# Kernel optimization log

Measured on AMD Instinct MI355X. Metric: run time of the kernel, lower is better.

Reference implementation:

```python
import jax, jax.numpy as jnp
import numpy as np

D = 64        # inner_feature_len (dim)
HID = 128     # hidden_channels of the edge MLP
NCONV = 2     # n_conv
STEPS = 3     # Set2Set processing_steps
NSEG = 128    # number of graphs in the batch


def setup_inputs() -> dict:
    key = jax.random.key(0)
    ks = jax.random.split(key, 30)
    N, E, FN, FE = 10000, 64000, 92, 41
    s = 0.05
    p = lambda i, shape: jax.random.normal(ks[i], shape, jnp.float32) * s
    return {
        "x": jax.random.normal(ks[0], (N, FN), jnp.float32),
        "edge_attr": jax.random.uniform(ks[1], (E, FE), dtype=jnp.float32),
        "lin0_w": p(2, (D, FN)), "lin0_b": p(3, (D,)),
        "nn1_w": p(4, (HID, FE)), "nn1_b": p(5, (HID,)),
        "nn2_w": p(6, (D * D, HID)), "nn2_b": p(7, (D * D,)),
        "root_w": p(8, (D, D)), "conv_b": p(9, (D,)),
        "gru_w_ih": p(10, (3 * D, D)), "gru_w_hh": p(11, (3 * D, D)),
        "gru_b_ih": p(12, (3 * D,)), "gru_b_hh": p(13, (3 * D,)),
        "lstm_w_ih": p(14, (4 * D, 2 * D)), "lstm_w_hh": p(15, (4 * D, D)),
        "lstm_b_ih": p(16, (4 * D,)), "lstm_b_hh": p(17, (4 * D,)),
        "lin1_w": p(18, (D, 2 * D)), "lin1_b": p(19, (D,)),
        "lin2_w": p(20, (1, D)), "lin2_b": p(21, (1,)),
        "edge_index": jax.random.randint(ks[22], (2, E), 0, N, dtype=jnp.int32),
        "batch": jnp.sort(jax.random.randint(ks[23], (N,), 0, NSEG, dtype=jnp.int32)),
    }


def _gru_step(m, h, w_ih, w_hh, b_ih, b_hh):
    # torch GRU gate order: r, z, n
    gi = m @ w_ih.T + b_ih
    gh = h @ w_hh.T + b_hh
    r = jax.nn.sigmoid(gi[:, :D] + gh[:, :D])
    z = jax.nn.sigmoid(gi[:, D:2 * D] + gh[:, D:2 * D])
    n = jnp.tanh(gi[:, 2 * D:] + r * gh[:, 2 * D:])
    return (1.0 - z) * n + z * h


def _forward(x, edge_attr, lin0_w, lin0_b, nn1_w, nn1_b, nn2_w, nn2_b, root_w, conv_b,
             gru_w_ih, gru_w_hh, gru_b_ih, gru_b_hh, lstm_w_ih, lstm_w_hh, lstm_b_ih,
             lstm_b_hh, lin1_w, lin1_b, lin2_w, lin2_b, edge_index, batch):
    N = x.shape[0]
    src, dst = edge_index[0], edge_index[1]

    # Edge-conditioned weight matrices: [E, D, D] (dominant intermediate)
    We = (jax.nn.relu(edge_attr @ nn1_w.T + nn1_b) @ nn2_w.T + nn2_b).reshape(-1, D, D)
    deg = jnp.clip(jax.ops.segment_sum(jnp.ones_like(src, jnp.float32), dst, num_segments=N), 1.0, None)

    out = jax.nn.relu(x @ lin0_w.T + lin0_b)   # [N, D]
    h = out                                     # GRU hidden (num_layers=1)
    for _ in range(NCONV):
        # NNConv: gather -> per-edge matmul -> scatter-mean, plus root transform + bias
        msg = jnp.einsum('ei,eio->eo', out[src], We)                 # [E, D]
        agg = jax.ops.segment_sum(msg, dst, num_segments=N) / deg[:, None]
        m = jax.nn.relu(agg + out @ root_w.T + conv_b)
        h = _gru_step(m, h, gru_w_ih, gru_w_hh, gru_b_ih, gru_b_hh)
        out = h

    # Set2Set pooling (LSTM-attention readout)
    q_star = jnp.zeros((NSEG, 2 * D), x.dtype)
    hl = jnp.zeros((NSEG, D), x.dtype)
    cl = jnp.zeros((NSEG, D), x.dtype)
    for _ in range(STEPS):
        g = q_star @ lstm_w_ih.T + lstm_b_ih + hl @ lstm_w_hh.T + lstm_b_hh
        i = jax.nn.sigmoid(g[:, :D])
        f = jax.nn.sigmoid(g[:, D:2 * D])
        gg = jnp.tanh(g[:, 2 * D:3 * D])
        o = jax.nn.sigmoid(g[:, 3 * D:])
        cl = f * cl + i * gg
        hl = o * jnp.tanh(cl)
        q = hl                                   # [NSEG, D]
        e = jnp.sum(out * q[batch], axis=-1)     # [N]
        mmax = jax.ops.segment_max(e, batch, num_segments=NSEG)
        a = jnp.exp(e - mmax[batch])
        denom = jax.ops.segment_sum(a, batch, num_segments=NSEG)
        a = a / denom[batch]
        r = jax.ops.segment_sum(a[:, None] * out, batch, num_segments=NSEG)  # [NSEG, D]
        q_star = jnp.concatenate([q, r], axis=1)

    y = jax.nn.relu(q_star @ lin1_w.T + lin1_b) @ lin2_w.T + lin2_b
    return y.reshape(-1)


def reference(x, edge_attr, lin0_w, lin0_b, nn1_w, nn1_b, nn2_w, nn2_b, root_w, conv_b,
              gru_w_ih, gru_w_hh, gru_b_ih, gru_b_hh, lstm_w_ih, lstm_w_hh, lstm_b_ih,
              lstm_b_hh, lin1_w, lin1_b, lin2_w, lin2_b, edge_index, batch):
    return _forward(x, edge_attr, lin0_w, lin0_b, nn1_w, nn1_b, nn2_w, nn2_b, root_w,
                    conv_b, gru_w_ih, gru_w_hh, gru_b_ih, gru_b_hh, lstm_w_ih, lstm_w_hh,
                    lstm_b_ih, lstm_b_hh, lin1_w, lin1_b, lin2_w, lin2_b, edge_index, batch)
```

## Files before the change

kernel.cpp:

```cpp
#include <hip/hip_runtime.h>
#include <hip/hip_bf16.h>
#include <math.h>

#define DD 64
#define HIDC 128
#define FN 92
#define FE 41
#define S2CAP 192

typedef unsigned short u16;
typedef short bf16x8 __attribute__((ext_vector_type(8)));
typedef float f32x4 __attribute__((ext_vector_type(4)));
typedef u16 u16x8 __attribute__((ext_vector_type(8)));

__device__ __forceinline__ float sigmoidf_(float x){ return 1.f/(1.f+expf(-x)); }

__device__ __forceinline__ u16 f2bf(float v){
  union { float f; unsigned u; } x; x.f = v;
  unsigned r = x.u + 0x7fff + ((x.u >> 16) & 1);
  return (u16)(r >> 16);
}
__device__ __forceinline__ float bf2f(u16 v){
  union { float f; unsigned u; } x; x.u = ((unsigned)v) << 16;
  return x.f;
}
__device__ __forceinline__ void split_bf(float v, u16& h, u16& l){
  h = f2bf(v); l = f2bf(v - bf2f(h));
}

__global__ void k_pack(const float* __restrict__ lin0_w, const float* __restrict__ nn1_w,
                       const float* __restrict__ root_w, const float* __restrict__ gwih,
                       const float* __restrict__ gwhh, const float* __restrict__ lwih,
                       const float* __restrict__ lwhh, const float* __restrict__ lin1_w,
                       float* __restrict__ lin0T, float* __restrict__ nn1T,
                       float* __restrict__ rootT, float* __restrict__ wihT,
                       float* __restrict__ whhT, float* __restrict__ lwihT,
                       float* __restrict__ lwhhT, float* __restrict__ lin1T)
{
  int idx = blockIdx.x*blockDim.x + threadIdx.x;
  if (idx < 92*64){ int k=idx/64, o=idx%64; lin0T[k*64+o] = lin0_w[o*92+k]; return; } idx -= 92*64;
  if (idx < 41*128){ int k=idx/128, h=idx%128; nn1T[k*128+h] = nn1_w[h*41+k]; return; } idx -= 41*128;
  if (idx < 64*64){ int i=idx/64, o=idx%64; rootT[i*64+o] = root_w[o*64+i]; return; } idx -= 64*64;
  if (idx < 64*192){ int i=idx/192, g=idx%192; wihT[i*192+g] = gwih[g*64+i]; return; } idx -= 64*192;
  if (idx < 64*192){ int i=idx/192, g=idx%192; whhT[i*192+g] = gwhh[g*64+i]; return; } idx -= 64*192;
  if (idx < 128*256){ int j=idx/256, t=idx%256; lwihT[j*256+t] = lwih[t*128+j]; return; } idx -= 128*256;
  if (idx < 64*256){ int j=idx/256, t=idx%256; lwhhT[j*256+t] = lwhh[t*64+j]; return; } idx -= 64*256;
  if (idx < 128*64){ int j=idx/64, t=idx%64; lin1T[j*64+t] = lin1_w[t*128+j]; return; }
}

__global__ void k_pack_b2(const float* __restrict__ nn2_w,
                          u16* __restrict__ BhT, u16* __restrict__ BlT){
  int idx = blockIdx.x*256 + threadIdx.x;
  if (idx >= 524288) return;
  int i  = idx & 63;
  int ho = (idx >> 6) & 4095;
  int c  = idx >> 18;
  int h = ho >> 6, o = ho & 63;
  float v = nn2_w[(size_t)(i*64+o)*128 + c*64 + h];
  u16 hi, lo; split_bf(v, hi, lo);
  BhT[idx] = hi; BlT[idx] = lo;
}

__global__ void k_pack_b1(const float* __restrict__ nn1_w,
                          u16* __restrict__ BT1h, u16* __restrict__ BT1l){
  int idx = blockIdx.x*256 + threadIdx.x;
  if (idx >= 8192) return;
  int h = idx >> 6, k = idx & 63;
  float v = (k < FE) ? nn1_w[(size_t)h*FE + k] : 0.f;
  u16 hi, lo; split_bf(v, hi, lo);
  BT1h[idx] = hi; BT1l[idx] = lo;
}

__global__ void k_split_ea(const float* __restrict__ ea, const int* __restrict__ sortedE,
                           u16* __restrict__ eaH, u16* __restrict__ eaL, int E){
  int idx = blockIdx.x*256 + threadIdx.x;
  if (idx >= E*64) return;
  int ew = idx >> 6, k = idx & 63;
  int e = sortedE[ew];
  float v = (k < FE) ? ea[(size_t)e*FE + k] : 0.f;
  u16 hi, lo; split_bf(v, hi, lo);
  eaH[idx] = hi; eaL[idx] = lo;
}

__global__ __launch_bounds__(256) void k_node_mlp(const float* __restrict__ x,
    const float* __restrict__ lin0T, const float* __restrict__ lin0_b,
    const float* __restrict__ nn2_b,
    float* __restrict__ out, u16* __restrict__ outH, u16* __restrict__ outL,
    float* __restrict__ bterm, int N)
{
  __shared__ float xs[4][FN];
  int base = blockIdx.x*4;
  for (int i=threadIdx.x; i<4*FN; i+=256){
    int n = base + i/FN;
    xs[i/FN][i%FN] = (n<N) ? x[(size_t)n*FN + i%FN] : 0.f;
  }
  __syncthreads();
  int ln = threadIdx.x>>6, o = threadIdx.x&63;
  int n = base+ln;
  if (n>=N) return;
  float acc = lin0_b[o];
  #pragma unroll 4
  for (int k=0;k<FN;k++) acc = fmaf(xs[ln][k], lin0T[k*64+o], acc);
  float v = fmaxf(acc, 0.f);
  out[(size_t)n*64+o] = v;
  u16 hi, lo; split_bf(v, hi, lo);
  outH[(size_t)n*64+o] = hi;
  outL[(size_t)n*64+o] = lo;
  float bt = 0.f;
  #pragma unroll 8
  for (int i=0;i<64;i++) bt = fmaf(__shfl(v, i, 64), nn2_b[i*64+o], bt);
  bterm[(size_t)n*64+o] = bt;
}

__global__ void k_count(const int* __restrict__ dst, const int* __restrict__ src,
                        float* __restrict__ deg, int* __restrict__ scnt, int E){
  int e = blockIdx.x*blockDim.x + threadIdx.x;
  if (e < E){
    atomicAdd(&deg[dst[e]], 1.f);
    atomicAdd(&scnt[src[e]], 1);
  }
}

__global__ void k_scan1(const int* __restrict__ cnt, int* __restrict__ excl,
                        int* __restrict__ bsum, int N){
  __shared__ int buf[256];
  int i = blockIdx.x*256 + threadIdx.x;
  int v = (i<N) ? cnt[i] : 0;
  buf[threadIdx.x] = v;
  __syncthreads();
  #pragma unroll
  for (int off=1; off<256; off<<=1){
    int t = (threadIdx.x>=off) ? buf[threadIdx.x-off] : 0;
    __syncthreads();
    buf[threadIdx.x] += t;
    __syncthreads();
  }
  if (i<N) excl[i] = buf[threadIdx.x] - v;
  if (threadIdx.x==255) bsum[blockIdx.x] = buf[255];
}
__global__ void k_scan2(int* __restrict__ bsum, int nb){
  __shared__ int buf[256];
  int v = (threadIdx.x<nb) ? bsum[threadIdx.x] : 0;
  buf[threadIdx.x] = v;
  __syncthreads();
  #pragma unroll
  for (int off=1; off<256; off<<=1){
    int t = (threadIdx.x>=off) ? buf[threadIdx.x-off] : 0;
    __syncthreads();
    buf[threadIdx.x] += t;
    __syncthreads();
  }
  if (threadIdx.x<nb) bsum[threadIdx.x] = buf[threadIdx.x] - v;
}
__global__ void k_scan3(int* __restrict__ starts, int* __restrict__ cursor,
                        const int* __restrict__ bsum, int N, int E){
  int i = blockIdx.x*256 + threadIdx.x;
  if (i<N){
    int s = starts[i] + bsum[blockIdx.x];
    starts[i] = s;
    cursor[i] = s;
  }
  if (i==0) starts[N] = E;
}

__global__ void k_sort(const int* __restrict__ src, const int* __restrict__ dst,
                       int* __restrict__ cursor, int* __restrict__ sortedE,
                       int* __restrict__ srcS, int* __restrict__ dstS, int E){
  int e = blockIdx.x*256 + threadIdx.x;
  if (e < E){
    int s = src[e];
    int p = atomicAdd(&cursor[s], 1);
    sortedE[p] = e;
    srcS[p] = s;
    dstS[p] = dst[e];
  }
}

__global__ __launch_bounds__(256,3) void k_edge_mlp_mfma(
    const u16* __restrict__ eaH, const u16* __restrict__ eaL,
    const u16* __restrict__ BT1h, const u16* __restrict__ BT1l,
    const float* __restrict__ nn1_b, float* __restrict__ hidden, int E)
{
  const int lane = threadIdx.x & 63;
  const int wave = threadIdx.x >> 6;
  const int row  = lane & 15;
  const int quad = lane >> 4;
  const int m0 = blockIdx.x*128 + (wave>>1)*64;
  const int n0 = (wave&1)*64;

  bf16x8 AH0[4], AH1[4], AL0[4], AL1[4];
  #pragma unroll
  for (int p=0;p<4;p++){
    int ar = min(m0 + p*16 + row, E-1);
    const u16* aH = eaH + (size_t)ar*64 + quad*8;
    const u16* aL = eaL + (size_t)ar*64 + quad*8;
    AH0[p] = *(const bf16x8*)(aH);
    AH1[p] = *(const bf16x8*)(aH + 32);
    AL0[p] = *(const bf16x8*)(aL);
    AL1[p] = *(const bf16x8*)(aL + 32);
  }
  #pragma unroll
  for (int tb=0;tb<4;tb++){
    const u16* bH = BT1h + (size_t)(n0 + tb*16 + row)*64 + quad*8;
    const u16* bL = BT1l + (size_t)(n0 + tb*16 + row)*64 + quad*8;
    bf16x8 bh0 = *(const bf16x8*)(bH);
    bf16x8 bh1 = *(const bf16x8*)(bH + 32);
    bf16x8 bl0 = *(const bf16x8*)(bL);
    bf16x8 bl1 = *(const bf16x8*)(bL + 32);
    float4 bias;
    {
      int nb = n0 + tb*16 + quad*4;
      bias.x = nn1_b[nb+0]; bias.y = nn1_b[nb+1];
      bias.z = nn1_b[nb+2]; bias.w = nn1_b[nb+3];
    }
    #pragma unroll
    for (int ta=0;ta<4;ta++){
      f32x4 a = {0.f,0.f,0.f,0.f};
      a = __builtin_amdgcn_mfma_f32_16x16x32_bf16(bh0, AH0[ta], a, 0,0,0);
      a = __builtin_amdgcn_mfma_f32_16x16x32_bf16(bh1, AH1[ta], a, 0,0,0);
      a = __builtin_amdgcn_mfma_f32_16x16x32_bf16(bl0, AH0[ta], a, 0,0,0);
      a = __builtin_amdgcn_mfma_f32_16x16x32_bf16(bl1, AH1[ta], a, 0,0,0);
      a = __builtin_amdgcn_mfma_f32_16x16x32_bf16(bh0, AL0[ta], a, 0,0,0);
      a = __builtin_amdgcn_mfma_f32_16x16x32_bf16(bh1, AL1[ta], a, 0,0,0);
      int m = m0 + ta*16 + row;
      if (m < E){
        float4 v;
        v.x = fmaxf(a[0]+bias.x, 0.f); v.y = fmaxf(a[1]+bias.y, 0.f);
        v.z = fmaxf(a[2]+bias.z, 0.f); v.w = fmaxf(a[3]+bias.w, 0.f);
        *(float4*)(hidden + (size_t)m*128 + n0 + tb*16 + quad*4) = v;
      }
    }
  }
}

__global__ __launch_bounds__(256,3) void k_qgemm_mfma(
    const u16* __restrict__ Ah, const u16* __restrict__ Al,
    const u16* __restrict__ BhT, const u16* __restrict__ BlT,
    u16* __restrict__ C, int M)
{
  const int lane = threadIdx.x & 63;
  const int wave = threadIdx.x >> 6;
  const int row  = lane & 15;
  const int quad = lane >> 4;
  const int m0 = blockIdx.y * 64;
  const int n0 = blockIdx.x * 256 + wave * 64;

  bf16x8 AH0[4], AH1[4], AL0[4], AL1[4];
  #pragma unroll
  for (int p=0;p<4;p++){
    int ar = min(m0 + p*16 + row, M-1);
    const u16* aH = Ah + (size_t)ar*64 + quad*8;
    const u16* aL = Al + (size_t)ar*64 + quad*8;
    AH0[p] = *(const bf16x8*)(aH);
    AH1[p] = *(const bf16x8*)(aH + 32);
    AL0[p] = *(const bf16x8*)(aL);
    AL1[p] = *(const bf16x8*)(aL + 32);
  }

  f32x4 acc[4][4];
  #pragma unroll
  for (int ta=0;ta<4;ta++)
    #pragma unroll
    for (int tb=0;tb<4;tb++)
      acc[ta][tb] = (f32x4){0.f,0.f,0.f,0.f};

  #pragma unroll
  for (int tb=0;tb<4;tb++){
    const u16* bH = BhT + (size_t)(n0 + tb*16 + row)*64 + quad*8;
    const u16* bL = BlT + (size_t)(n0 + tb*16 + row)*64 + quad*8;
    bf16x8 bh0 = *(const bf16x8*)(bH);
    bf16x8 bh1 = *(const bf16x8*)(bH + 32);
    bf16x8 bl0 = *(const bf16x8*)(bL);
    bf16x8 bl1 = *(const bf16x8*)(bL + 32);
    #pragma unroll
    for (int ta=0;ta<4;ta++){
      f32x4 a = acc[ta][tb];
      a = __builtin_amdgcn_mfma_f32_16x16x32_bf16(bh0, AH0[ta], a, 0,0,0);
      a = __builtin_amdgcn_mfma_f32_16x16x32_bf16(bh1, AH1[ta], a, 0,0,0);
      a = __builtin_amdgcn_mfma_f32_16x16x32_bf16(bl0, AH0[ta], a, 0,0,0);
      a = __builtin_amdgcn_mfma_f32_16x16x32_bf16(bl1, AH1[ta], a, 0,0,0);
      a = __builtin_amdgcn_mfma_f32_16x16x32_bf16(bh0, AL0[ta], a, 0,0,0);
      a = __builtin_amdgcn_mfma_f32_16x16x32_bf16(bh1, AL1[ta], a, 0,0,0);
      acc[ta][tb] = a;
    }
  }

  #pragma unroll
  for (int ta=0;ta<4;ta++){
    int m = m0 + ta*16 + row;
    if (m >= M) continue;
    u16* dst = C + (size_t)m*4096 + n0 + quad*8;
    #pragma unroll
    for (int p=0;p<2;p++){
      f32x4 aa = acc[ta][2*p];
      f32x4 ab = acc[ta][2*p+1];
      u16x8 v;
      v[0]=f2bf(aa[0]); v[1]=f2bf(aa[1]); v[2]=f2bf(aa[2]); v[3]=f2bf(aa[3]);
      v[4]=f2bf(ab[0]); v[5]=f2bf(ab[1]); v[6]=f2bf(ab[2]); v[7]=f2bf(ab[3]);
      *(u16x8*)(dst + p*32) = v;
    }
  }
}

template<int PASS>
__global__ __launch_bounds__(256) void k_edge_gather(const u16* __restrict__ Q,
    const float* __restrict__ hidden, int h0,
    const float* __restrict__ bterm, const int* __restrict__ srcS,
    const int* __restrict__ dstS,
    float* __restrict__ msg, float* __restrict__ agg, int E)
{
  __shared__ float hs[4][2][64];
  __shared__ float red[4][2][64];
  const int wv = threadIdx.x>>6, lane = threadIdx.x&63;
  const int ew0 = (blockIdx.x*4 + wv)*2;
  const bool v0 = (ew0 < E), v1 = (ew0+1 < E);
  const int e0 = v0 ? ew0 : 0;
  const int e1 = v1 ? ew0+1 : 0;
  const int s0 = srcS[e0], s1 = srcS[e1];
  hs[wv][0][lane] = hidden[(size_t)e0*128 + h0 + lane];
  hs[wv][1][lane] = hidden[(size_t)e1*128 + h0 + lane];
  const int sg = lane>>4, oq = lane&15;
  const int posb = ((oq>>3)<<5) + ((oq&3)<<3) + (((oq>>2)&1)<<2);
  const u16* q0 = Q + (size_t)s0*4096 + sg*64 + posb;
  const u16* q1 = Q + (size_t)s1*4096 + sg*64 + posb;
  float a00=0.f,a01=0.f,a02=0.f,a03=0.f;
  float a10=0.f,a11=0.f,a12=0.f,a13=0.f;
  #pragma unroll
  for (int j=0;j<16;j++){
    ushort4 qa = *(const ushort4*)(q0 + j*256);
    ushort4 qb = *(const ushort4*)(q1 + j*256);
    float h0v = hs[wv][0][j*4 + sg];
    float h1v = hs[wv][1][j*4 + sg];
    a00 = fmaf(h0v, bf2f(qa.x), a00); a01 = fmaf(h0v, bf2f(qa.y), a01);
    a02 = fmaf(h0v, bf2f(qa.z), a02); a03 = fmaf(h0v, bf2f(qa.w), a03);
    a10 = fmaf(h1v, bf2f(qb.x), a10); a11 = fmaf(h1v, bf2f(qb.y), a11);
    a12 = fmaf(h1v, bf2f(qb.z), a12); a13 = fmaf(h1v, bf2f(qb.w), a13);
  }
  a00 += __shfl_xor(a00,16); a00 += __shfl_xor(a00,32);
  a01 += __shfl_xor(a01,16); a01 += __shfl_xor(a01,32);
  a02 += __shfl_xor(a02,16); a02 += __shfl_xor(a02,32);
  a03 += __shfl_xor(a03,16); a03 += __shfl_xor(a03,32);
  a10 += __shfl_xor(a10,16); a10 += __shfl_xor(a10,32);
  a11 += __shfl_xor(a11,16); a11 += __shfl_xor(a11,32);
  a12 += __shfl_xor(a12,16); a12 += __shfl_xor(a12,32);
  a13 += __shfl_xor(a13,16); a13 += __shfl_xor(a13,32);
  if (lane < 16){
    float4 r0; r0.x=a00; r0.y=a01; r0.z=a02; r0.w=a03;
    float4 r1; r1.x=a10; r1.y=a11; r1.z=a12; r1.w=a13;
    *(float4*)&red[wv][0][lane*4] = r0;
    *(float4*)&red[wv][1][lane*4] = r1;
  }
  if (v0){
    float rv = red[wv][0][lane];
    if (PASS == 0) msg[(size_t)ew0*64 + lane] = bterm[(size_t)s0*64 + lane] + rv;
    else atomicAdd(&agg[(size_t)dstS[ew0]*64 + lane], msg[(size_t)ew0*64 + lane] + rv);
  }
  if (v1){
    float rv = red[wv][1][lane];
    if (PASS == 0) msg[(size_t)(ew0+1)*64 + lane] = bterm[(size_t)s1*64 + lane] + rv;
    else atomicAdd(&agg[(size_t)dstS[ew0+1]*64 + lane], msg[(size_t)(ew0+1)*64 + lane] + rv);
  }
}

__global__ __launch_bounds__(256) void k_node_update(const float* __restrict__ outOld,
    const float* __restrict__ agg, const float* __restrict__ deg,
    const float* __restrict__ rootT, const float* __restrict__ conv_b,
    const float* __restrict__ wihT, const float* __restrict__ whhT,
    const float* __restrict__ b_ih, const float* __restrict__ b_hh,
    const float* __restrict__ nn2_b,
    float* __restrict__ outNew, u16* __restrict__ outH, u16* __restrict__ outL,
    float* __restrict__ bterm, int N)
{
  __shared__ float hs[4][64];
  __shared__ float ms[4][64];
  int ln = threadIdx.x>>6, o = threadIdx.x&63;
  int n = blockIdx.x*4+ln;
  bool ok = (n<N);
  float h = ok ? outOld[(size_t)n*64+o] : 0.f;
  hs[ln][o] = h;
  __syncthreads();
  float root = 0.f;
  #pragma unroll 8
  for (int i=0;i<64;i++) root = fmaf(hs[ln][i], rootT[i*64+o], root);
  float d = ok ? fmaxf(deg[n], 1.f) : 1.f;
  float a = ok ? agg[(size_t)n*64+o]/d : 0.f;
  float m = fmaxf(a + root + conv_b[o], 0.f);
  ms[ln][o] = m;
  __syncthreads();
  float gir=b_ih[o], giz=b_ih[64+o], gin=b_ih[128+o];
  float ghr=b_hh[o], ghz=b_hh[64+o], ghn=b_hh[128+o];
  #pragma unroll 4
  for (int i=0;i<64;i++){
    float mi = ms[ln][i], hi = hs[ln][i];
    gir = fmaf(mi, wihT[i*192+o],      gir);
    giz = fmaf(mi, wihT[i*192+64+o],   giz);
    gin = fmaf(mi, wihT[i*192+128+o],  gin);
    ghr = fmaf(hi, whhT[i*192+o],      ghr);
    ghz = fmaf(hi, whhT[i*192+64+o],   ghz);
    ghn = fmaf(hi, whhT[i*192+128+o],  ghn);
  }
  float r = sigmoidf_(gir+ghr);
  float z = sigmoidf_(giz+ghz);
  float nn = tanhf(gin + r*ghn);
  if (ok){
    float v = (1.f-z)*nn + z*h;
    outNew[(size_t)n*64+o] = v;
    u16 hi16, lo16; split_bf(v, hi16, lo16);
    outH[(size_t)n*64+o] = hi16;
    outL[(size_t)n*64+o] = lo16;
    float bt = 0.f;
    #pragma unroll 8
    for (int i=0;i<64;i++) bt = fmaf(__shfl(v, i, 64), nn2_b[i*64+o], bt);
    bterm[(size_t)n*64+o] = bt;
  }
}

__global__ __launch_bounds__(256) void k_set2set(const float* __restrict__ out,
    const int* __restrict__ batch, int N,
    const float* __restrict__ lwihT, const float* __restrict__ lwhhT,
    const float* __restrict__ b_ih, const float* __restrict__ b_hh,
    const float* __restrict__ lin1T, const float* __restrict__ lin1_b,
    const float* __restrict__ lin2_w, const float* __restrict__ lin2_b,
    float* __restrict__ y)
{
  __shared__ float X[S2CAP][65];
  __shared__ float earr[S2CAP];
  __shared__ float qstar[128], hl[64], cl[64], g[256];
  __shared__ float rpart[4][64], spart[4], redm[4], zs[64];
  __shared__ int sb[2];
  const int tid = threadIdx.x;
  const int b = blockIdx.x;
  const int wid = tid>>6, lane = tid&63;
  if (tid < 128) qstar[tid] = 0.f;
  if (tid < 64){ hl[tid]=0.f; cl[tid]=0.f; }
  if (tid == 0){
    int lo=0, hi=N;
    while (lo<hi){ int mid=(lo+hi)>>1; if (batch[mid] < b) lo=mid+1; else hi=mid; }
    sb[0]=lo;
    int lo2=lo, hi2=N;
    while (lo2<hi2){ int mid=(lo2+hi2)>>1; if (batch[mid] < b+1) lo2=mid+1; else hi2=mid; }
    sb[1]=lo2;
  }
  __syncthreads();
  const int nlo = sb[0], nhi = sb[1], nn = nhi - nlo;
  const bool single = (nn <= S2CAP);
  if (single){
    for (int idx = tid; idx < nn*64; idx += 256){
      X[idx>>6][idx&63] = out[(size_t)(nlo + (idx>>6))*64 + (idx&63)];
    }
  }
  __syncthreads();

  for (int step=0; step<3; step++){
    float gs = b_ih[tid] + b_hh[tid];
    for (int j=0;j<128;j++) gs = fmaf(qstar[j], lwihT[j*256+tid], gs);
    for (int j=0;j<64;j++)  gs = fmaf(hl[j],    lwhhT[j*256+tid], gs);
    g[tid] = gs;
    __syncthreads();
    if (tid < 64){
      float ig = sigmoidf_(g[tid]);
      float fg = sigmoidf_(g[64+tid]);
      float gg = tanhf(g[128+tid]);
      float og = sigmoidf_(g[192+tid]);
      float c = fg*cl[tid] + ig*gg;
      cl[tid] = c;
      hl[tid] = og*tanhf(c);
    }
    __syncthreads();

    if (single){
      float lm = -INFINITY;
      for (int n = tid; n < nn; n += 256){
        float acc = 0.f;
        #pragma unroll 8
        for (int d=0; d<64; d++) acc = fmaf(X[n][d], hl[d], acc);
        earr[n] = acc;
        lm = fmaxf(lm, acc);
      }
      lm = fmaxf(lm, __shfl_xor(lm,1));  lm = fmaxf(lm, __shfl_xor(lm,2));
      lm = fmaxf(lm, __shfl_xor(lm,4));  lm = fmaxf(lm, __shfl_xor(lm,8));
      lm = fmaxf(lm, __shfl_xor(lm,16)); lm = fmaxf(lm, __shfl_xor(lm,32));
      if (lane==0) redm[wid] = lm;
      __syncthreads();
      if (tid==0) redm[0] = fmaxf(fmaxf(redm[0],redm[1]), fmaxf(redm[2],redm[3]));
      __syncthreads();
      const float gmax = redm[0];
      float ls = 0.f;
      for (int n = tid; n < nn; n += 256){
        float a = expf(earr[n] - gmax);
        earr[n] = a;
        ls += a;
      }
      ls += __shfl_xor(ls,1);  ls += __shfl_xor(ls,2);  ls += __shfl_xor(ls,4);
      ls += __shfl_xor(ls,8);  ls += __shfl_xor(ls,16); ls += __shfl_xor(ls,32);
      if (lane==0) spart[wid] = ls;
      __syncthreads();
      float racc = 0.f;
      for (int n = wid; n < nn; n += 4) racc = fmaf(earr[n], X[n][lane], racc);
      rpart[wid][lane] = racc;
      __syncthreads();
      if (tid < 64){
        float r = rpart[0][tid]+rpart[1][tid]+rpart[2][tid]+rpart[3][tid];
        float s = spart[0]+spart[1]+spart[2]+spart[3];
        qstar[tid] = hl[tid];
        qstar[64+tid] = (nn>0) ? r/s : 0.f;
      }
      __syncthreads();
    } else {
      float qv = hl[lane];
      float lm = -INFINITY;
      for (int n = nlo + wid; n < nhi; n += 4){
        float p = out[(size_t)n*64 + lane]*qv;
        p += __shfl_xor(p,1); p += __shfl_xor(p,2); p += __shfl_xor(p,4);
        p += __shfl_xor(p,8); p += __shfl_xor(p,16); p += __shfl_xor(p,32);
        lm = fmaxf(lm, p);
      }
      if (lane==0) redm[wid] = lm;
      __syncthreads();
      if (tid==0) redm[0] = fmaxf(fmaxf(redm[0],redm[1]), fmaxf(redm[2],redm[3]));
      __syncthreads();
      float gmax = redm[0];
      float sw = 0.f, racc = 0.f;
      for (int n = nlo + wid; n < nhi; n += 4){
        float ol = out[(size_t)n*64 + lane];
        float p = ol*qv;
        p += __shfl_xor(p,1); p += __shfl_xor(p,2); p += __shfl_xor(p,4);
        p += __shfl_xor(p,8); p += __shfl_xor(p,16); p += __shfl_xor(p,32);
        float a = expf(p - gmax);
        sw += a;
        racc = fmaf(a, ol, racc);
      }
      rpart[wid][lane] = racc;
      if (lane==0) spart[wid] = sw;
      __syncthreads();
      if (tid < 64){
        float r = rpart[0][tid]+rpart[1][tid]+rpart[2][tid]+rpart[3][tid];
        float s = spart[0]+spart[1]+spart[2]+spart[3];
        qstar[tid] = hl[tid];
        qstar[64+tid] = (nn>0) ? r/s : 0.f;
      }
      __syncthreads();
    }
  }
  if (tid < 64){
    float acc = lin1_b[tid];
    for (int j=0;j<128;j++) acc = fmaf(qstar[j], lin1T[j*64+tid], acc);
    zs[tid] = fmaxf(acc, 0.f);
  }
  __syncthreads();
  if (tid < 64){
    float v = zs[lane]*lin2_w[lane];
    v += __shfl_xor(v,1); v += __shfl_xor(v,2); v += __shfl_xor(v,4);
    v += __shfl_xor(v,8); v += __shfl_xor(v,16); v += __shfl_xor(v,32);
    if (lane==0) y[b] = v + lin2_b[0];
  }
}

extern "C" void kernel_launch(void* const* d_in, const int* in_sizes, int n_in,
                              void* d_out, int out_size, void* d_ws, size_t ws_size,
                              hipStream_t stream)
{
  const float* x      = (const float*)d_in[0];
  const float* eattr  = (const float*)d_in[1];
  const float* lin0_w = (const float*)d_in[2];
  const float* lin0_b = (const float*)d_in[3];
  const float* nn1_w  = (const float*)d_in[4];
  const float* nn1_b  = (const float*)d_in[5];
  const float* nn2_w  = (const float*)d_in[6];
  const float* nn2_b  = (const float*)d_in[7];
  const float* root_w = (const float*)d_in[8];
  const float* conv_b = (const float*)d_in[9];
  const float* gwih   = (const float*)d_in[10];
  const float* gwhh   = (const float*)d_in[11];
  const float* gbih   = (const float*)d_in[12];
  const float* gbhh   = (const float*)d_in[13];
  const float* lwih   = (const float*)d_in[14];
  const float* lwhh   = (const float*)d_in[15];
  const float* lbih   = (const float*)d_in[16];
  const float* lbhh   = (const float*)d_in[17];
  const float* lin1_w = (const float*)d_in[18];
  const float* lin1_b = (const float*)d_in[19];
  const float* lin2_w = (const float*)d_in[20];
  const float* lin2_b = (const float*)d_in[21];
  const int*   eidx   = (const int*)d_in[22];
  const int*   batch  = (const int*)d_in[23];

  const int N = in_sizes[0]/FN;
  const int E = in_sizes[1]/FE;
  const int* srcI = eidx;
  const int* dstI = eidx + E;

  char* w = (char*)d_ws;
  size_t off = 0;
  auto alloc = [&](size_t bytes)->char* {
    char* p = w + off;
    off = (off + bytes + 255) & ~(size_t)255;
    return p;
  };
  float* degw  = (float*)alloc((size_t)N*4);
  int*   scnt  = (int*)alloc((size_t)N*4);
  int*   starts= (int*)alloc((size_t)(N+1)*4);
  int*   cursor= (int*)alloc((size_t)N*4);
  int*   bsum  = (int*)alloc((size_t)256*4);
  int*   sortedE=(int*)alloc((size_t)E*4);
  int*   srcS  = (int*)alloc((size_t)E*4);
  int*   dstS  = (int*)alloc((size_t)E*4);
  float* outA  = (float*)alloc((size_t)N*64*4);
  float* outB  = (float*)alloc((size_t)N*64*4);
  u16*   outAH = (u16*)alloc((size_t)N*64*2);
  u16*   outAL = (u16*)alloc((size_t)N*64*2);
  u16*   outBH = (u16*)alloc((size_t)N*64*2);
  u16*   outBL = (u16*)alloc((size_t)N*64*2);
  float* agg   = (float*)alloc((size_t)N*64*4);
  float* bterm = (float*)alloc((size_t)N*64*4);
  float* hidden= (float*)alloc((size_t)E*128*4);
  float* msg   = (float*)alloc((size_t)E*64*4);
  u16*   B2hT  = (u16*)alloc((size_t)524288*2);
  u16*   B2lT  = (u16*)alloc((size_t)524288*2);
  u16*   BT1h  = (u16*)alloc((size_t)8192*2);
  u16*   BT1l  = (u16*)alloc((size_t)8192*2);
  float* lin0T = (float*)alloc((size_t)92*64*4);
  float* nn1T  = (float*)alloc((size_t)41*128*4);
  float* rootT = (float*)alloc((size_t)64*64*4);
  float* wihT  = (float*)alloc((size_t)64*192*4);
  float* whhT  = (float*)alloc((size_t)64*192*4);
  float* lwihT = (float*)alloc((size_t)128*256*4);
  float* lwhhT = (float*)alloc((size_t)64*256*4);
  float* lin1T = (float*)alloc((size_t)128*64*4);
  u16*   Q     = (u16*)alloc((size_t)N*4096*2);
  u16* eaH = (u16*)Q;
  u16* eaL = eaH + (size_t)E*64;

  const int NB = (N+255)/256;

  hipMemsetAsync(degw, 0, (size_t)N*4, stream);
  hipMemsetAsync(scnt, 0, (size_t)N*4, stream);
  k_pack<<<(97152+255)/256, 256, 0, stream>>>(lin0_w, nn1_w, root_w, gwih, gwhh,
      lwih, lwhh, lin1_w, lin0T, nn1T, rootT, wihT, whhT, lwihT, lwhhT, lin1T);
  k_pack_b2<<<524288/256, 256, 0, stream>>>(nn2_w, B2hT, B2lT);
  k_pack_b1<<<8192/256, 256, 0, stream>>>(nn1_w, BT1h, BT1l);
  k_node_mlp<<<(N+3)/4, 256, 0, stream>>>(x, lin0T, lin0_b, nn2_b, outA, outAH, outAL, bterm, N);
  k_count<<<(E+255)/256, 256, 0, stream>>>(dstI, srcI, degw, scnt, E);
  k_scan1<<<NB, 256, 0, stream>>>(scnt, starts, bsum, N);
  k_scan2<<<1, 256, 0, stream>>>(bsum, NB);
  k_scan3<<<NB, 256, 0, stream>>>(starts, cursor, bsum, N, E);
  k_sort<<<(E+255)/256, 256, 0, stream>>>(srcI, dstI, cursor, sortedE, srcS, dstS, E);
  k_split_ea<<<((size_t)E*64+255)/256, 256, 0, stream>>>(eattr, sortedE, eaH, eaL, E);
  k_edge_mlp_mfma<<<(E+127)/128, 256, 0, stream>>>(eaH, eaL, BT1h, BT1l, nn1_b, hidden, E);

  float* cur = outA; float* nxt = outB;
  u16* curH = outAH; u16* curL = outAL;
  u16* nxtH = outBH; u16* nxtL = outBL;
  const dim3 qgrid(16, (N+63)/64);
  const int gatherGx = (E+7)/8;
  for (int conv=0; conv<2; conv++){
    hipMemsetAsync(agg, 0, (size_t)N*64*4, stream);
    k_qgemm_mfma<<<qgrid, 256, 0, stream>>>(curH, curL, B2hT, B2lT, Q, N);
    k_edge_gather<0><<<gatherGx, 256, 0, stream>>>(Q, hidden, 0, bterm, srcS, dstS, msg, agg, E);
    k_qgemm_mfma<<<qgrid, 256, 0, stream>>>(curH, curL, B2hT + 262144, B2lT + 262144, Q, N);
    k_edge_gather<1><<<gatherGx, 256, 0, stream>>>(Q, hidden, 64, bterm, srcS, dstS, msg, agg, E);
    k_node_update<<<(N+3)/4, 256, 0, stream>>>(cur, agg, degw, rootT, conv_b,
        wihT, whhT, gbih, gbhh, nn2_b, nxt, nxtH, nxtL, bterm, N);
    float* t = cur; cur = nxt; nxt = t;
    u16* th = curH; curH = nxtH; nxtH = th;
    u16* tl = curL; curL = nxtL; nxtL = tl;
  }

  k_set2set<<<128, 256, 0, stream>>>(cur, batch, N, lwihT, lwhhT, lbih, lbhh,
      lin1T, lin1_b, lin2_w, lin2_b, (float*)d_out);
}
```

Baseline: 623.8 us.

## Gather edges per source node, keep Q slice in registers, drop msg buffer

The edge gather kernel now assigns one wave per source node and walks its CSR edge range. The node's 64x64 Q slice is loaded once into registers and reused for every outgoing edge, instead of being reloaded from global memory per edge. Each pass now atomically adds its partial message, with the bias term added in pass 0, directly into agg. This removes the intermediate msg array and the srcS array. The cost is load imbalance across nodes with different degrees, a serial per-edge loop with an LDS round trip, and twice as many atomics, since both passes now issue them.

```diff
diff --git a/kernel.cpp b/kernel.cpp
--- a/kernel.cpp
+++ b/kernel.cpp
@@ -165,13 +165,12 @@
 
 __global__ void k_sort(const int* __restrict__ src, const int* __restrict__ dst,
                        int* __restrict__ cursor, int* __restrict__ sortedE,
-                       int* __restrict__ srcS, int* __restrict__ dstS, int E){
+                       int* __restrict__ dstS, int E){
   int e = blockIdx.x*256 + threadIdx.x;
   if (e < E){
     int s = src[e];
     int p = atomicAdd(&cursor[s], 1);
     sortedE[p] = e;
-    srcS[p] = s;
     dstS[p] = dst[e];
   }
 }
@@ -305,60 +304,52 @@
 template<int PASS>
 __global__ __launch_bounds__(256) void k_edge_gather(const u16* __restrict__ Q,
     const float* __restrict__ hidden, int h0,
-    const float* __restrict__ bterm, const int* __restrict__ srcS,
-    const int* __restrict__ dstS,
-    float* __restrict__ msg, float* __restrict__ agg, int E)
-{
-  __shared__ float hs[4][2][64];
-  __shared__ float red[4][2][64];
+    const float* __restrict__ bterm, const int* __restrict__ starts,
+    const int* __restrict__ dstS, float* __restrict__ agg, int N)
+{
+  __shared__ float hs[4][64];
+  __shared__ float red[4][64];
   const int wv = threadIdx.x>>6, lane = threadIdx.x&63;
-  const int ew0 = (blockIdx.x*4 + wv)*2;
-  const bool v0 = (ew0 < E), v1 = (ew0+1 < E);
-  const int e0 = v0 ? ew0 : 0;
-  const int e1 = v1 ? ew0+1 : 0;
-  const int s0 = srcS[e0], s1 = srcS[e1];
-  hs[wv][0][lane] = hidden[(size_t)e0*128 + h0 + lane];
-  hs[wv][1][lane] = hidden[(size_t)e1*128 + h0 + lane];
+  const int n = blockIdx.x*4 + wv;
+  if (n >= N) return;
+  const int e0 = starts[n], e1 = starts[n+1];
+  if (e0 >= e1) return;
   const int sg = lane>>4, oq = lane&15;
   const int posb = ((oq>>3)<<5) + ((oq&3)<<3) + (((oq>>2)&1)<<2);
-  const u16* q0 = Q + (size_t)s0*4096 + sg*64 + posb;
-  const u16* q1 = Q + (size_t)s1*4096 + sg*64 + posb;
-  float a00=0.f,a01=0.f,a02=0.f,a03=0.f;
-  float a10=0.f,a11=0.f,a12=0.f,a13=0.f;
-  #pragma unroll
-  for (int j=0;j<16;j++){
-    ushort4 qa = *(const ushort4*)(q0 + j*256);
-    ushort4 qb = *(const ushort4*)(q1 + j*256);
-    float h0v = hs[wv][0][j*4 + sg];
-    float h1v = hs[wv][1][j*4 + sg];
-    a00 = fmaf(h0v, bf2f(qa.x), a00); a01 = fmaf(h0v, bf2f(qa.y), a01);
-    a02 = fmaf(h0v, bf2f(qa.z), a02); a03 = fmaf(h0v, bf2f(qa.w), a03);
-    a10 = fmaf(h1v, bf2f(qb.x), a10); a11 = fmaf(h1v, bf2f(qb.y), a11);
-    a12 = fmaf(h1v, bf2f(qb.z), a12); a13 = fmaf(h1v, bf2f(qb.w), a13);
-  }
-  a00 += __shfl_xor(a00,16); a00 += __shfl_xor(a00,32);
-  a01 += __shfl_xor(a01,16); a01 += __shfl_xor(a01,32);
-  a02 += __shfl_xor(a02,16); a02 += __shfl_xor(a02,32);
-  a03 += __shfl_xor(a03,16); a03 += __shfl_xor(a03,32);
-  a10 += __shfl_xor(a10,16); a10 += __shfl_xor(a10,32);
-  a11 += __shfl_xor(a11,16); a11 += __shfl_xor(a11,32);
-  a12 += __shfl_xor(a12,16); a12 += __shfl_xor(a12,32);
-  a13 += __shfl_xor(a13,16); a13 += __shfl_xor(a13,32);
-  if (lane < 16){
-    float4 r0; r0.x=a00; r0.y=a01; r0.z=a02; r0.w=a03;
-    float4 r1; r1.x=a10; r1.y=a11; r1.z=a12; r1.w=a13;
-    *(float4*)&red[wv][0][lane*4] = r0;
-    *(float4*)&red[wv][1][lane*4] = r1;
-  }
-  if (v0){
-    float rv = red[wv][0][lane];
-    if (PASS == 0) msg[(size_t)ew0*64 + lane] = bterm[(size_t)s0*64 + lane] + rv;
-    else atomicAdd(&agg[(size_t)dstS[ew0]*64 + lane], msg[(size_t)ew0*64 + lane] + rv);
-  }
-  if (v1){
-    float rv = red[wv][1][lane];
-    if (PASS == 0) msg[(size_t)(ew0+1)*64 + lane] = bterm[(size_t)s1*64 + lane] + rv;
-    else atomicAdd(&agg[(size_t)dstS[ew0+1]*64 + lane], msg[(size_t)(ew0+1)*64 + lane] + rv);
+  const u16* qp = Q + (size_t)n*4096 + sg*64 + posb;
+  ushort4 qreg[16];
+  #pragma unroll
+  for (int j=0;j<16;j++) qreg[j] = *(const ushort4*)(qp + j*256);
+  const float bt = (PASS==0) ? bterm[(size_t)n*64 + lane] : 0.f;
+
+  float hvN = hidden[(size_t)e0*128 + h0 + lane];
+  int   dN  = dstS[e0];
+  for (int e=e0; e<e1; ++e){
+    const float hv = hvN;
+    const int   d  = dN;
+    if (e+1 < e1){
+      hvN = hidden[(size_t)(e+1)*128 + h0 + lane];
+      dN  = dstS[e+1];
+    }
+    hs[wv][lane] = hv;
+    float a0=0.f,a1=0.f,a2=0.f,a3=0.f;
+    #pragma unroll
+    for (int j=0;j<16;j++){
+      float h4 = hs[wv][j*4+sg];
+      a0 = fmaf(h4, bf2f(qreg[j].x), a0);
+      a1 = fmaf(h4, bf2f(qreg[j].y), a1);
+      a2 = fmaf(h4, bf2f(qreg[j].z), a2);
+      a3 = fmaf(h4, bf2f(qreg[j].w), a3);
+    }
+    a0 += __shfl_xor(a0,16); a0 += __shfl_xor(a0,32);
+    a1 += __shfl_xor(a1,16); a1 += __shfl_xor(a1,32);
+    a2 += __shfl_xor(a2,16); a2 += __shfl_xor(a2,32);
+    a3 += __shfl_xor(a3,16); a3 += __shfl_xor(a3,32);
+    if (lane < 16){
+      float4 r; r.x=a0; r.y=a1; r.z=a2; r.w=a3;
+      *(float4*)&red[wv][lane*4] = r;
+    }
+    atomicAdd(&agg[(size_t)d*64 + lane], bt + red[wv][lane]);
   }
 }
 
@@ -603,7 +594,6 @@
   int*   cursor= (int*)alloc((size_t)N*4);
   int*   bsum  = (int*)alloc((size_t)256*4);
   int*   sortedE=(int*)alloc((size_t)E*4);
-  int*   srcS  = (int*)alloc((size_t)E*4);
   int*   dstS  = (int*)alloc((size_t)E*4);
   float* outA  = (float*)alloc((size_t)N*64*4);
   float* outB  = (float*)alloc((size_t)N*64*4);
@@ -614,7 +604,6 @@
   float* agg   = (float*)alloc((size_t)N*64*4);
   float* bterm = (float*)alloc((size_t)N*64*4);
   float* hidden= (float*)alloc((size_t)E*128*4);
-  float* msg   = (float*)alloc((size_t)E*64*4);
   u16*   B2hT  = (u16*)alloc((size_t)524288*2);
   u16*   B2lT  = (u16*)alloc((size_t)524288*2);
   u16*   BT1h  = (u16*)alloc((size_t)8192*2);
@@ -644,7 +633,7 @@
   k_scan1<<<NB, 256, 0, stream>>>(scnt, starts, bsum, N);
   k_scan2<<<1, 256, 0, stream>>>(bsum, NB);
   k_scan3<<<NB, 256, 0, stream>>>(starts, cursor, bsum, N, E);
-  k_sort<<<(E+255)/256, 256, 0, stream>>>(srcI, dstI, cursor, sortedE, srcS, dstS, E);
+  k_sort<<<(E+255)/256, 256, 0, stream>>>(srcI, dstI, cursor, sortedE, dstS, E);
   k_split_ea<<<((size_t)E*64+255)/256, 256, 0, stream>>>(eattr, sortedE, eaH, eaL, E);
   k_edge_mlp_mfma<<<(E+127)/128, 256, 0, stream>>>(eaH, eaL, BT1h, BT1l, nn1_b, hidden, E);
 
@@ -652,13 +641,13 @@
   u16* curH = outAH; u16* curL = outAL;
   u16* nxtH = outBH; u16* nxtL = outBL;
   const dim3 qgrid(16, (N+63)/64);
-  const int gatherGx = (E+7)/8;
+  const int gatherG = (N+3)/4;
   for (int conv=0; conv<2; conv++){
     hipMemsetAsync(agg, 0, (size_t)N*64*4, stream);
     k_qgemm_mfma<<<qgrid, 256, 0, stream>>>(curH, curL, B2hT, B2lT, Q, N);
-    k_edge_gather<0><<<gatherGx, 256, 0, stream>>>(Q, hidden, 0, bterm, srcS, dstS, msg, agg, E);
+    k_edge_gather<0><<<gatherG, 256, 0, stream>>>(Q, hidden, 0, bterm, starts, dstS, agg, N);
     k_qgemm_mfma<<<qgrid, 256, 0, stream>>>(curH, curL, B2hT + 262144, B2lT + 262144, Q, N);
-    k_edge_gather<1><<<gatherGx, 256, 0, stream>>>(Q, hidden, 64, bterm, srcS, dstS, msg, agg, E);
+    k_edge_gather<1><<<gatherG, 256, 0, stream>>>(Q, hidden, 64, bterm, starts, dstS, agg, N);
     k_node_update<<<(N+3)/4, 256, 0, stream>>>(cur, agg, degw, rootT, conv_b,
         wihT, whhT, gbih, gbhh, nn2_b, nxt, nxtH, nxtL, bterm, N);
     float* t = cur; cur = nxt; nxt = t;
```

New measurement: 573.4 us. 1.09x faster.
